# Performance work log

Hardware: AMD Instinct MI355X
Metric: run time of the kernel (lower is better)

Reference implementation:

```python
import jax, jax.numpy as jnp
import numpy as np

N = 50000          # nodes
E = 800000         # edges (avg degree 16)
D = 128            # feature dim
MSG_EPS = 1e-7     # GENConv eps added to relu(msg)
SM_EPS = 1e-16     # pyg softmax denominator eps
BN_EPS = 1e-5
LN_EPS = 1e-5


def setup_inputs() -> dict:
    key = jax.random.key(0)
    ks = jax.random.split(key, 6)
    x = jax.random.normal(ks[0], (N, D), dtype=jnp.float32)
    edge_index = jax.random.randint(ks[1], (2, E), 0, N, dtype=jnp.int32)
    t = jnp.array(1.0, dtype=jnp.float32)
    W1 = jax.random.normal(ks[2], (D, 2 * D), dtype=jnp.float32) / np.sqrt(D).astype(np.float32)
    b1 = jnp.zeros((2 * D,), jnp.float32)
    bn_gamma = jnp.ones((2 * D,), jnp.float32)
    bn_beta = jnp.zeros((2 * D,), jnp.float32)
    W2 = jax.random.normal(ks[3], (2 * D, D), dtype=jnp.float32) / np.sqrt(2 * D).astype(np.float32)
    b2 = jnp.zeros((D,), jnp.float32)
    ln_gamma = jnp.ones((D,), jnp.float32)
    ln_beta = jnp.zeros((D,), jnp.float32)
    return {"x": x, "edge_index": edge_index, "t": t, "W1": W1, "b1": b1,
            "bn_gamma": bn_gamma, "bn_beta": bn_beta, "W2": W2, "b2": b2,
            "ln_gamma": ln_gamma, "ln_beta": ln_beta}


def reference(x, edge_index, t, W1, b1, bn_gamma, bn_beta, W2, b2, ln_gamma, ln_beta):
    src, dst = edge_index[0], edge_index[1]
    # --- GENConv message: relu(x_j) + eps  -> [E, D]
    msg = jax.nn.relu(x[src]) + MSG_EPS
    # --- softmax aggregation over incoming edges per dst node, per feature
    logits = t * msg                                            # [E, D]
    seg_max = jax.ops.segment_max(logits, dst, num_segments=N)  # [N, D]
    seg_max = jnp.where(jnp.isfinite(seg_max), seg_max, 0.0)    # empty segments -> 0
    ex = jnp.exp(logits - seg_max[dst])                         # [E, D]
    denom = jax.ops.segment_sum(ex, dst, num_segments=N)        # [N, D]
    alpha = ex / (denom[dst] + SM_EPS)                          # [E, D]
    agg = jax.ops.segment_sum(alpha * msg, dst, num_segments=N) # [N, D]
    # --- GENConv update: MLP(agg + x), MLP = Lin(D,2D)->BN->ReLU->Lin(2D,D)
    h = agg + x
    h = h @ W1 + b1                                             # [N, 2D]
    mu = jnp.mean(h, axis=0)
    var = jnp.var(h, axis=0)
    h = (h - mu) * jax.lax.rsqrt(var + BN_EPS) * bn_gamma + bn_beta
    h = jax.nn.relu(h)
    h = h @ W2 + b2                                             # [N, D]
    # --- LayerNorm -> ReLU -> (dropout p=0 noop) -> residual
    mu2 = jnp.mean(h, axis=-1, keepdims=True)
    var2 = jnp.mean(jnp.square(h - mu2), axis=-1, keepdims=True)
    h = (h - mu2) * jax.lax.rsqrt(var2 + LN_EPS) * ln_gamma + ln_beta
    h = jax.nn.relu(h)
    return x + h
```

## Files before the change

### kernel.cpp

```cpp
#include <hip/hip_runtime.h>

#define D 128
#define D2 256
#define BSH 5
#define BNODES 32
#define NBMAX 2048
#define CAP 640
#define PCHUNK 4096

typedef __attribute__((ext_vector_type(8))) short short8;
typedef __attribute__((ext_vector_type(4))) float f32x4;

__device__ inline unsigned short f2b(float f) {
  unsigned u = __float_as_uint(f);
  unsigned r = (u + 0x7FFFu + ((u >> 16) & 1u)) >> 16;
  return (unsigned short)r;
}
__device__ inline float b2f(unsigned short h) {
  return __uint_as_float(((unsigned)h) << 16);
}
__device__ inline float lo2f(unsigned u) { return __uint_as_float(u << 16); }
__device__ inline float hi2f(unsigned u) { return __uint_as_float(u & 0xffff0000u); }

__global__ void convert_w_kernel(const float* __restrict__ W1,
                                 const float* __restrict__ W2,
                                 unsigned short* __restrict__ W1f,
                                 unsigned short* __restrict__ W2f) {
  int idx = blockIdx.x * 256 + threadIdx.x;
  if (idx < 32768) {
    int k = idx >> 8, n = idx & 255;
    int t = n >> 4, m16 = n & 15;
    int kk = k >> 5, quad = (k >> 3) & 3, j = k & 7;
    W1f[(((t * 4 + kk) * 64 + quad * 16 + m16) << 3) + j] = f2b(W1[idx]);
  } else {
    int i = idx - 32768;
    int k = i >> 7, n = i & 127;
    int t = n >> 4, m16 = n & 15;
    int kk = k >> 5, quad = (k >> 3) & 3, j = k & 7;
    W2f[(((t * 8 + kk) * 64 + quad * 16 + m16) << 3) + j] = f2b(W2[i]);
  }
}

__global__ void mb_kernel(const float* __restrict__ x, unsigned short* __restrict__ mb,
                          int total4) {
  int i = blockIdx.x * 256 + threadIdx.x;
  if (i < total4) {
    float4 v = reinterpret_cast<const float4*>(x)[i];
    unsigned lo = (unsigned)f2b(fmaxf(v.x, 0.f) + 1e-7f) |
                  ((unsigned)f2b(fmaxf(v.y, 0.f) + 1e-7f) << 16);
    unsigned hi = (unsigned)f2b(fmaxf(v.z, 0.f) + 1e-7f) |
                  ((unsigned)f2b(fmaxf(v.w, 0.f) + 1e-7f) << 16);
    reinterpret_cast<uint2*>(mb)[i] = make_uint2(lo, hi);
  } else if (i < total4 + 32) {
    reinterpret_cast<uint2*>(mb)[i] = make_uint2(0u, 0u);
  }
}

__global__ __launch_bounds__(256) void part_kernel(const int* __restrict__ ei,
                                                   int* __restrict__ cursor,
                                                   unsigned* __restrict__ pairbuf,
                                                   int E, int nb) {
  __shared__ int cnt[NBMAX];
  __shared__ int base[NBMAX];
  int tid = threadIdx.x;
  int c0 = blockIdx.x * PCHUNK;
  int nE = min(PCHUNK, E - c0);
  for (int i = tid; i < nb; i += 256) cnt[i] = 0;
  __syncthreads();
  for (int j = tid; j < nE; j += 256) {
    int dst = ei[E + c0 + j];
    atomicAdd(&cnt[dst >> BSH], 1);
  }
  __syncthreads();
  for (int i = tid; i < nb; i += 256) {
    int c = cnt[i];
    base[i] = (c > 0) ? atomicAdd(&cursor[i], c) : 0;
    cnt[i] = 0;
  }
  __syncthreads();
  for (int j = tid; j < nE; j += 256) {
    int e = c0 + j;
    int dst = ei[E + e];
    int src = ei[e];
    int b = dst >> BSH;
    int r = base[b] + atomicAdd(&cnt[b], 1);
    if (r < CAP)
      pairbuf[(size_t)b * CAP + r] =
          (unsigned)src | ((unsigned)(dst & (BNODES - 1)) << 16);
  }
}

__global__ __launch_bounds__(256) void agg2_kernel(const float* __restrict__ x,
                                                   const unsigned short* __restrict__ mb,
                                                   const unsigned* __restrict__ pairbuf,
                                                   const int* __restrict__ cursor,
                                                   const float* __restrict__ tptr,
                                                   unsigned short* __restrict__ h0b, int N) {
  __shared__ unsigned spair[CAP];
  __shared__ unsigned short ssrc[CAP + 8 * BNODES];
  __shared__ int cnt[BNODES], off[BNODES], run[BNODES], pcnt[BNODES];
  int b = blockIdx.x;
  int tid = threadIdx.x;
  int Eb = min(cursor[b], CAP);
  if (tid < BNODES) { cnt[tid] = 0; run[tid] = 0; }
  __syncthreads();
  for (int j = tid; j < Eb; j += 256) {
    unsigned p = pairbuf[(size_t)b * CAP + j];
    spair[j] = p;
    atomicAdd(&cnt[p >> 16], 1);
  }
  __syncthreads();
  if (tid < BNODES) {
    int c = cnt[tid];
    int pc = (c + 7) & ~7;
    pcnt[tid] = pc;
    int s = pc;
#pragma unroll
    for (int st = 1; st < 32; st <<= 1) {
      int u = __shfl_up(s, st, 32);
      if ((tid & 31) >= st) s += u;
    }
    off[tid] = s - pc;
  }
  __syncthreads();
  for (int j = tid; j < Eb; j += 256) {
    unsigned p = spair[j];
    int dl = p >> 16;
    int r = atomicAdd(&run[dl], 1);
    ssrc[off[dl] + r] = (unsigned short)(p & 0xffffu);
  }
  if (tid < BNODES) {
    int o = off[tid];
    for (int r = cnt[tid]; r < pcnt[tid]; ++r) ssrc[o + r] = (unsigned short)N;
  }
  __syncthreads();

  int w = tid >> 6;
  int l = tid & 63;
  float t = tptr[0];
  const unsigned short* mbc = mb + 2 * l;
  for (int ln = w; ln < BNODES; ln += 4) {
    int n = (b << BSH) + ln;
    if (n >= N) continue;
    int s0 = off[ln];
    int dn = pcnt[ln];
    float fnpad = (float)(dn - cnt[ln]);
    float den0 = 0.f, num0 = 0.f, den1 = 0.f, num1 = 0.f;
    for (int j = 0; j < dn; j += 8) {
      unsigned uu[8];
#pragma unroll
      for (int q = 0; q < 8; ++q) {
        int aq = ssrc[s0 + j + q];
        uu[q] = *reinterpret_cast<const unsigned*>(mbc + ((size_t)aq << 7));
      }
#pragma unroll
      for (int q = 0; q < 8; ++q) {
        float m0 = lo2f(uu[q]);
        float m1 = hi2f(uu[q]);
        float e0 = __expf(t * m0);
        float e1 = __expf(t * m1);
        den0 += e0; num0 += e0 * m0;
        den1 += e1; num1 += e1 * m1;
      }
    }
    den0 -= fnpad;
    den1 -= fnpad;
    size_t idx = ((size_t)n << 7) + 2 * l;
    float2 xv = *reinterpret_cast<const float2*>(x + idx);
    float v0 = num0 / (den0 + 1e-16f) + xv.x;
    float v1 = num1 / (den1 + 1e-16f) + xv.y;
    *reinterpret_cast<unsigned*>(h0b + idx) =
        (unsigned)f2b(v0) | ((unsigned)f2b(v1) << 16);
  }
}

__global__ __launch_bounds__(256) void gemm1_mfma(
    const unsigned short* __restrict__ h0b, const unsigned short* __restrict__ W1f,
    unsigned short* __restrict__ h1b,
    float* __restrict__ bnsum, float* __restrict__ bnsumsq, int M) {
  __shared__ unsigned short lt[4][64][72];
  int tid = threadIdx.x;
  int w = tid >> 6;
  int l = tid & 63;
  int m16 = l & 15;
  int quad = l >> 4;
  int r0 = blockIdx.x * 64;

  f32x4 acc[4][4];
#pragma unroll
  for (int rt = 0; rt < 4; ++rt)
#pragma unroll
    for (int ct = 0; ct < 4; ++ct) acc[rt][ct] = (f32x4){0.f, 0.f, 0.f, 0.f};

#pragma unroll
  for (int kk = 0; kk < 4; ++kk) {
    short8 bfr[4];
#pragma unroll
    for (int ct = 0; ct < 4; ++ct)
      bfr[ct] = *reinterpret_cast<const short8*>(
          W1f + ((((w * 4 + ct) * 4 + kk) * 64 + l) << 3));
    short8 a[4];
#pragma unroll
    for (int rt = 0; rt < 4; ++rt) {
      int row = min(r0 + rt * 16 + m16, M - 1);
      a[rt] = *reinterpret_cast<const short8*>(h0b + (size_t)row * D + kk * 32 + quad * 8);
    }
#pragma unroll
    for (int rt = 0; rt < 4; ++rt)
#pragma unroll
      for (int ct = 0; ct < 4; ++ct)
        acc[rt][ct] = __builtin_amdgcn_mfma_f32_16x16x32_bf16(a[rt], bfr[ct], acc[rt][ct], 0, 0, 0);
  }

#pragma unroll
  for (int ct = 0; ct < 4; ++ct) {
    int col = w * 64 + ct * 16 + m16;
    float cs = 0.f, cq = 0.f;
#pragma unroll
    for (int rt = 0; rt < 4; ++rt) {
      int rloc = rt * 16 + quad * 4;
#pragma unroll
      for (int reg = 0; reg < 4; ++reg) {
        float val = acc[rt][ct][reg];
        if (r0 + rloc + reg < M) {
          cs += val;
          cq += val * val;
        }
        lt[w][rloc + reg][ct * 16 + m16] = f2b(val);
      }
    }
    cs += __shfl_xor(cs, 16, 64);
    cs += __shfl_xor(cs, 32, 64);
    cq += __shfl_xor(cq, 16, 64);
    cq += __shfl_xor(cq, 32, 64);
    if (quad == 0) {
      atomicAdd(&bnsum[col], cs);
      atomicAdd(&bnsumsq[col], cq);
    }
  }

  int row = r0 + l;
  if (row < M) {
    const unsigned short* src = &lt[w][l][0];
    unsigned short* dst = h1b + (size_t)row * D2 + w * 64;
#pragma unroll
    for (int j = 0; j < 8; ++j)
      *reinterpret_cast<short8*>(dst + j * 8) =
          *reinterpret_cast<const short8*>(src + j * 8);
  }
}

__global__ void bnfinal_kernel(const float* __restrict__ bnsum,
                               const float* __restrict__ bnsumsq,
                               const float* __restrict__ gamma,
                               const float* __restrict__ beta,
                               float* __restrict__ scale,
                               float* __restrict__ shift, int M) {
  int c = threadIdx.x;
  float invM = 1.f / (float)M;
  float mu = bnsum[c] * invM;
  float var = bnsumsq[c] * invM - mu * mu;
  float sc = gamma[c] * rsqrtf(var + 1e-5f);
  scale[c] = sc;
  shift[c] = beta[c] - mu * sc;
}

__global__ __launch_bounds__(256) void bnapply_kernel(
    unsigned short* __restrict__ h1b, const float* __restrict__ scale,
    const float* __restrict__ shift, int total8) {
  int i = blockIdx.x * 256 + threadIdx.x;
  if (i >= total8) return;
  int c0 = (i << 3) & 255;
  f32x4 sc0 = *reinterpret_cast<const f32x4*>(scale + c0);
  f32x4 sc1 = *reinterpret_cast<const f32x4*>(scale + c0 + 4);
  f32x4 sh0 = *reinterpret_cast<const f32x4*>(shift + c0);
  f32x4 sh1 = *reinterpret_cast<const f32x4*>(shift + c0 + 4);
  uint4 raw = reinterpret_cast<const uint4*>(h1b)[i];
  unsigned words[4] = {raw.x, raw.y, raw.z, raw.w};
  uint4 o;
  unsigned ow[4];
#pragma unroll
  for (int p = 0; p < 2; ++p) {
    f32x4 sc = p ? sc1 : sc0;
    f32x4 sh = p ? sh1 : sh0;
#pragma unroll
    for (int q = 0; q < 2; ++q) {
      unsigned u = words[p * 2 + q];
      float v0 = fmaxf(lo2f(u) * sc[q * 2] + sh[q * 2], 0.f);
      float v1 = fmaxf(hi2f(u) * sc[q * 2 + 1] + sh[q * 2 + 1], 0.f);
      ow[p * 2 + q] = (unsigned)f2b(v0) | ((unsigned)f2b(v1) << 16);
    }
  }
  o.x = ow[0]; o.y = ow[1]; o.z = ow[2]; o.w = ow[3];
  reinterpret_cast<uint4*>(h1b)[i] = o;
}

__global__ __launch_bounds__(256) void gemm2_mfma(
    const unsigned short* __restrict__ h1c, const unsigned short* __restrict__ W2f,
    const float* __restrict__ b2, const float* __restrict__ lng,
    const float* __restrict__ lnb, const float* __restrict__ x,
    float* __restrict__ out, int M) {
  __shared__ float lnp[128][2], lnp2[128][2];
  int tid = threadIdx.x;
  int w = tid >> 6;
  int l = tid & 63;
  int m16 = l & 15;
  int quad = l >> 4;
  int rb = w >> 1, cb = w & 1;
  int r00 = blockIdx.x * 128;

  f32x4 acc[4][4];
#pragma unroll
  for (int rt = 0; rt < 4; ++rt)
#pragma unroll
    for (int ct = 0; ct < 4; ++ct) acc[rt][ct] = (f32x4){0.f, 0.f, 0.f, 0.f};

#pragma unroll
  for (int kk = 0; kk < 8; ++kk) {
    short8 a[4];
#pragma unroll
    for (int rt = 0; rt < 4; ++rt) {
      int row = min(r00 + rb * 64 + rt * 16 + m16, M - 1);
      a[rt] = *reinterpret_cast<const short8*>(h1c + (size_t)row * D2 + kk * 32 + quad * 8);
    }
    short8 bfr[4];
#pragma unroll
    for (int ct = 0; ct < 4; ++ct)
      bfr[ct] = *reinterpret_cast<const short8*>(
          W2f + ((((cb * 4 + ct) * 8 + kk) * 64 + l) << 3));
#pragma unroll
    for (int rt = 0; rt < 4; ++rt)
#pragma unroll
      for (int ct = 0; ct < 4; ++ct)
        acc[rt][ct] = __builtin_amdgcn_mfma_f32_16x16x32_bf16(a[rt], bfr[ct], acc[rt][ct], 0, 0, 0);
  }

  float b2v[4], lgv[4], lbv[4];
#pragma unroll
  for (int ct = 0; ct < 4; ++ct) {
    int col = cb * 64 + ct * 16 + m16;
    b2v[ct] = b2[col];
    lgv[ct] = lng[col];
    lbv[ct] = lnb[col];
  }

#pragma unroll
  for (int rt = 0; rt < 4; ++rt) {
#pragma unroll
    for (int reg = 0; reg < 4; ++reg) {
      float s = 0.f, s2 = 0.f;
#pragma unroll
      for (int ct = 0; ct < 4; ++ct) {
        float v = acc[rt][ct][reg] + b2v[ct];
        s += v;
        s2 += v * v;
      }
#pragma unroll
      for (int msk = 1; msk < 16; msk <<= 1) {
        s += __shfl_xor(s, msk, 64);
        s2 += __shfl_xor(s2, msk, 64);
      }
      if (m16 == 0) {
        int rl = rb * 64 + rt * 16 + quad * 4 + reg;
        lnp[rl][cb] = s;
        lnp2[rl][cb] = s2;
      }
    }
  }
  __syncthreads();

#pragma unroll
  for (int rt = 0; rt < 4; ++rt) {
#pragma unroll
    for (int reg = 0; reg < 4; ++reg) {
      int rl = rb * 64 + rt * 16 + quad * 4 + reg;
      int row = r00 + rl;
      float s = lnp[rl][0] + lnp[rl][1];
      float s2 = lnp2[rl][0] + lnp2[rl][1];
      float mu = s * (1.f / 128.f);
      float var = s2 * (1.f / 128.f) - mu * mu;
      float inv = rsqrtf(var + 1e-5f);
      if (row < M) {
#pragma unroll
        for (int ct = 0; ct < 4; ++ct) {
          int col = cb * 64 + ct * 16 + m16;
          float v = acc[rt][ct][reg] + b2v[ct];
          float h = fmaxf((v - mu) * inv * lgv[ct] + lbv[ct], 0.f);
          out[(size_t)row * D + col] = x[(size_t)row * D + col] + h;
        }
      }
    }
  }
}

extern "C" void kernel_launch(void* const* d_in, const int* in_sizes, int n_in,
                              void* d_out, int out_size, void* d_ws, size_t ws_size,
                              hipStream_t stream) {
  const float* x   = (const float*)d_in[0];
  const int*   ei  = (const int*)d_in[1];
  const float* t   = (const float*)d_in[2];
  const float* W1  = (const float*)d_in[3];
  const float* bng = (const float*)d_in[5];
  const float* bnb = (const float*)d_in[6];
  const float* W2  = (const float*)d_in[7];
  const float* b2  = (const float*)d_in[8];
  const float* lng = (const float*)d_in[9];
  const float* lnb = (const float*)d_in[10];
  float* out = (float*)d_out;

  int N = in_sizes[0] / D;
  int E = in_sizes[1] / 2;
  size_t nd = (size_t)N * D;
  int nb = (N + BNODES - 1) >> BSH;

  unsigned short* mb  = (unsigned short*)d_ws;
  unsigned short* h0b = mb + nd + 128;
  unsigned short* h1b = h0b + nd;
  unsigned short* W1f = h1b + 2 * nd;
  unsigned short* W2f = W1f + 32768;
  float* bnsum   = (float*)(W2f + 32768);
  float* bnsumsq = bnsum + D2;
  float* bnscale = bnsumsq + D2;
  float* bnshift = bnscale + D2;
  int* cursor = (int*)(bnshift + D2);
  unsigned* pairbuf = (unsigned*)(cursor + NBMAX);

  hipMemsetAsync(bnsum, 0, (4 * D2 + NBMAX) * sizeof(int), stream);

  convert_w_kernel<<<256, 256, 0, stream>>>(W1, W2, W1f, W2f);
  int total4 = (int)(nd / 4);
  mb_kernel<<<(total4 + 32 + 255) / 256, 256, 0, stream>>>(x, mb, total4);

  part_kernel<<<(E + PCHUNK - 1) / PCHUNK, 256, 0, stream>>>(ei, cursor, pairbuf, E, nb);
  agg2_kernel<<<nb, 256, 0, stream>>>(x, mb, pairbuf, cursor, t, h0b, N);

  gemm1_mfma<<<(N + 63) / 64, 256, 0, stream>>>(h0b, W1f, h1b, bnsum, bnsumsq, N);
  bnfinal_kernel<<<1, 256, 0, stream>>>(bnsum, bnsumsq, bng, bnb, bnscale, bnshift, N);
  int total8 = (int)(2 * nd / 8);
  bnapply_kernel<<<(total8 + 255) / 256, 256, 0, stream>>>(h1b, bnscale, bnshift, total8);
  gemm2_mfma<<<(N + 127) / 128, 256, 0, stream>>>(h1b, W2f, b2, lng, lnb, x, out, N);
}
```

Measured before the change: 231.7 us.

## Software-pipeline gather in aggregation, widen its blocks, and halve gemm2 row tile

Measured after the change: 225.1 us. -2.9%, faster.

```diff
diff --git a/kernel.cpp b/kernel.cpp
--- a/kernel.cpp
+++ b/kernel.cpp
@@ -90,29 +90,25 @@
   }
 }
 
-__global__ __launch_bounds__(256) void agg2_kernel(const float* __restrict__ x,
+__global__ __launch_bounds__(512) void agg2_kernel(const float* __restrict__ x,
                                                    const unsigned short* __restrict__ mb,
                                                    const unsigned* __restrict__ pairbuf,
                                                    const int* __restrict__ cursor,
                                                    const float* __restrict__ tptr,
                                                    unsigned short* __restrict__ h0b, int N) {
-  __shared__ unsigned spair[CAP];
-  __shared__ unsigned short ssrc[CAP + 8 * BNODES];
+  __shared__ int soff[CAP + 4 * BNODES];
   __shared__ int cnt[BNODES], off[BNODES], run[BNODES], pcnt[BNODES];
   int b = blockIdx.x;
   int tid = threadIdx.x;
   int Eb = min(cursor[b], CAP);
   if (tid < BNODES) { cnt[tid] = 0; run[tid] = 0; }
   __syncthreads();
-  for (int j = tid; j < Eb; j += 256) {
-    unsigned p = pairbuf[(size_t)b * CAP + j];
-    spair[j] = p;
-    atomicAdd(&cnt[p >> 16], 1);
-  }
+  for (int j = tid; j < Eb; j += 512)
+    atomicAdd(&cnt[pairbuf[(size_t)b * CAP + j] >> 16], 1);
   __syncthreads();
   if (tid < BNODES) {
     int c = cnt[tid];
-    int pc = (c + 7) & ~7;
+    int pc = (c + 3) & ~3;
     pcnt[tid] = pc;
     int s = pc;
 #pragma unroll
@@ -123,38 +119,53 @@
     off[tid] = s - pc;
   }
   __syncthreads();
-  for (int j = tid; j < Eb; j += 256) {
-    unsigned p = spair[j];
+  for (int j = tid; j < Eb; j += 512) {
+    unsigned p = pairbuf[(size_t)b * CAP + j];
     int dl = p >> 16;
     int r = atomicAdd(&run[dl], 1);
-    ssrc[off[dl] + r] = (unsigned short)(p & 0xffffu);
+    soff[off[dl] + r] = (int)(p & 0xffffu) << 8;
   }
   if (tid < BNODES) {
     int o = off[tid];
-    for (int r = cnt[tid]; r < pcnt[tid]; ++r) ssrc[o + r] = (unsigned short)N;
+    for (int r = cnt[tid]; r < pcnt[tid]; ++r) soff[o + r] = N << 8;
   }
   __syncthreads();
 
   int w = tid >> 6;
   int l = tid & 63;
   float t = tptr[0];
-  const unsigned short* mbc = mb + 2 * l;
-  for (int ln = w; ln < BNODES; ln += 4) {
+  int laneoff = l << 2;
+  const char* mbase = (const char*)mb;
+  for (int ln = w; ln < BNODES; ln += 8) {
     int n = (b << BSH) + ln;
     if (n >= N) continue;
     int s0 = off[ln];
     int dn = pcnt[ln];
-    float fnpad = (float)(dn - cnt[ln]);
     float den0 = 0.f, num0 = 0.f, den1 = 0.f, num1 = 0.f;
-    for (int j = 0; j < dn; j += 8) {
-      unsigned uu[8];
-#pragma unroll
-      for (int q = 0; q < 8; ++q) {
-        int aq = ssrc[s0 + j + q];
-        uu[q] = *reinterpret_cast<const unsigned*>(mbc + ((size_t)aq << 7));
-      }
-#pragma unroll
-      for (int q = 0; q < 8; ++q) {
+    if (dn > 0) {
+      unsigned uu[4];
+#pragma unroll
+      for (int q = 0; q < 4; ++q)
+        uu[q] = *(const unsigned*)(mbase + (soff[s0 + q] | laneoff));
+      for (int j = 4; j < dn; j += 4) {
+        unsigned vv[4];
+#pragma unroll
+        for (int q = 0; q < 4; ++q)
+          vv[q] = *(const unsigned*)(mbase + (soff[s0 + j + q] | laneoff));
+#pragma unroll
+        for (int q = 0; q < 4; ++q) {
+          float m0 = lo2f(uu[q]);
+          float m1 = hi2f(uu[q]);
+          float e0 = __expf(t * m0);
+          float e1 = __expf(t * m1);
+          den0 += e0; num0 += e0 * m0;
+          den1 += e1; num1 += e1 * m1;
+        }
+#pragma unroll
+        for (int q = 0; q < 4; ++q) uu[q] = vv[q];
+      }
+#pragma unroll
+      for (int q = 0; q < 4; ++q) {
         float m0 = lo2f(uu[q]);
         float m1 = hi2f(uu[q]);
         float e0 = __expf(t * m0);
@@ -162,9 +173,10 @@
         den0 += e0; num0 += e0 * m0;
         den1 += e1; num1 += e1 * m1;
       }
-    }
-    den0 -= fnpad;
-    den1 -= fnpad;
+      float fnpad = (float)(dn - cnt[ln]);
+      den0 -= fnpad;
+      den1 -= fnpad;
+    }
     size_t idx = ((size_t)n << 7) + 2 * l;
     float2 xv = *reinterpret_cast<const float2*>(x + idx);
     float v0 = num0 / (den0 + 1e-16f) + xv.x;
@@ -300,27 +312,27 @@
     const float* __restrict__ b2, const float* __restrict__ lng,
     const float* __restrict__ lnb, const float* __restrict__ x,
     float* __restrict__ out, int M) {
-  __shared__ float lnp[128][2], lnp2[128][2];
+  __shared__ float lnp[64][2], lnp2[64][2];
   int tid = threadIdx.x;
   int w = tid >> 6;
   int l = tid & 63;
   int m16 = l & 15;
   int quad = l >> 4;
   int rb = w >> 1, cb = w & 1;
-  int r00 = blockIdx.x * 128;
-
-  f32x4 acc[4][4];
-#pragma unroll
-  for (int rt = 0; rt < 4; ++rt)
+  int r00 = blockIdx.x * 64;
+
+  f32x4 acc[2][4];
+#pragma unroll
+  for (int rt = 0; rt < 2; ++rt)
 #pragma unroll
     for (int ct = 0; ct < 4; ++ct) acc[rt][ct] = (f32x4){0.f, 0.f, 0.f, 0.f};
 
 #pragma unroll
   for (int kk = 0; kk < 8; ++kk) {
-    short8 a[4];
-#pragma unroll
-    for (int rt = 0; rt < 4; ++rt) {
-      int row = min(r00 + rb * 64 + rt * 16 + m16, M - 1);
+    short8 a[2];
+#pragma unroll
+    for (int rt = 0; rt < 2; ++rt) {
+      int row = min(r00 + rb * 32 + rt * 16 + m16, M - 1);
       a[rt] = *reinterpret_cast<const short8*>(h1c + (size_t)row * D2 + kk * 32 + quad * 8);
     }
     short8 bfr[4];
@@ -329,7 +341,7 @@
       bfr[ct] = *reinterpret_cast<const short8*>(
           W2f + ((((cb * 4 + ct) * 8 + kk) * 64 + l) << 3));
 #pragma unroll
-    for (int rt = 0; rt < 4; ++rt)
+    for (int rt = 0; rt < 2; ++rt)
 #pragma unroll
       for (int ct = 0; ct < 4; ++ct)
         acc[rt][ct] = __builtin_amdgcn_mfma_f32_16x16x32_bf16(a[rt], bfr[ct], acc[rt][ct], 0, 0, 0);
@@ -345,7 +357,7 @@
   }
 
 #pragma unroll
-  for (int rt = 0; rt < 4; ++rt) {
+  for (int rt = 0; rt < 2; ++rt) {
 #pragma unroll
     for (int reg = 0; reg < 4; ++reg) {
       float s = 0.f, s2 = 0.f;
@@ -361,7 +373,7 @@
         s2 += __shfl_xor(s2, msk, 64);
       }
       if (m16 == 0) {
-        int rl = rb * 64 + rt * 16 + quad * 4 + reg;
+        int rl = rb * 32 + rt * 16 + quad * 4 + reg;
         lnp[rl][cb] = s;
         lnp2[rl][cb] = s2;
       }
@@ -370,10 +382,10 @@
   __syncthreads();
 
 #pragma unroll
-  for (int rt = 0; rt < 4; ++rt) {
+  for (int rt = 0; rt < 2; ++rt) {
 #pragma unroll
     for (int reg = 0; reg < 4; ++reg) {
-      int rl = rb * 64 + rt * 16 + quad * 4 + reg;
+      int rl = rb * 32 + rt * 16 + quad * 4 + reg;
       int row = r00 + rl;
       float s = lnp[rl][0] + lnp[rl][1];
       float s2 = lnp2[rl][0] + lnp2[rl][1];
@@ -432,11 +444,11 @@
   mb_kernel<<<(total4 + 32 + 255) / 256, 256, 0, stream>>>(x, mb, total4);
 
   part_kernel<<<(E + PCHUNK - 1) / PCHUNK, 256, 0, stream>>>(ei, cursor, pairbuf, E, nb);
-  agg2_kernel<<<nb, 256, 0, stream>>>(x, mb, pairbuf, cursor, t, h0b, N);
+  agg2_kernel<<<nb, 512, 0, stream>>>(x, mb, pairbuf, cursor, t, h0b, N);
 
   gemm1_mfma<<<(N + 63) / 64, 256, 0, stream>>>(h0b, W1f, h1b, bnsum, bnsumsq, N);
   bnfinal_kernel<<<1, 256, 0, stream>>>(bnsum, bnsumsq, bng, bnb, bnscale, bnshift, N);
   int total8 = (int)(2 * nd / 8);
   bnapply_kernel<<<(total8 + 255) / 256, 256, 0, stream>>>(h1b, bnscale, bnshift, total8);
-  gemm2_mfma<<<(N + 127) / 128, 256, 0, stream>>>(h1b, W2f, b2, lng, lnb, x, out, N);
-}
+  gemm2_mfma<<<(N + 63) / 64, 256, 0, stream>>>(h1b, W2f, b2, lng, lnb, x, out, N);
+}
```
